# Kernel tuning notes

Measured on AMD Instinct MI355X. Metric: run time of the kernel, lower is better.

Reference implementation:

```python
import jax, jax.numpy as jnp
import numpy as np

N_HEADS = 64
N_KV = 8
HEAD_DIM = 128
HIDDEN = 8192
BATCH = 32
PAD_LEN = 2048  # nearest_32(start_pos + 1) with start_pos = 2047


def setup_inputs() -> dict:
    key = jax.random.key(0)
    ks = jax.random.split(key, 8)
    w = 0.02
    return {
        "x": jax.random.normal(ks[0], (BATCH, 1, HIDDEN), jnp.float32),
        "wq": jax.random.normal(ks[1], (HIDDEN, N_HEADS * HEAD_DIM), jnp.float32) * w,
        "wk": jax.random.normal(ks[2], (HIDDEN, N_KV * HEAD_DIM), jnp.float32) * w,
        "wv": jax.random.normal(ks[3], (HIDDEN, N_KV * HEAD_DIM), jnp.float32) * w,
        "wo": jax.random.normal(ks[4], (N_HEADS * HEAD_DIM, HIDDEN), jnp.float32) * w,
        "rot_mat": jax.random.normal(ks[5], (HEAD_DIM, HEAD_DIM), jnp.float32) * w,
        "k_cache": jax.random.normal(ks[6], (BATCH, N_KV, PAD_LEN, HEAD_DIM), jnp.float32),
        "v_cache": jax.random.normal(ks[7], (BATCH, N_KV, PAD_LEN, HEAD_DIM), jnp.float32),
        "start_pos": 2047,
    }


def reference(x, wq, wk, wv, wo, rot_mat, k_cache, v_cache, start_pos):
    B = x.shape[0]
    L = k_cache.shape[2]  # padded past length (nearest_32(start_pos+1))
    scale = 1.0 / np.sqrt(HEAD_DIM).astype(np.float32)

    xt = x[:, 0]  # [B, HIDDEN], seq_len == 1 (decode)
    # QKV projections + rotary applied via explicit matmul with rot_mat
    q = (xt @ wq).reshape(B, N_HEADS, HEAD_DIM) @ rot_mat      # [B, nH, d]
    k_new = (xt @ wk).reshape(B, N_KV, HEAD_DIM) @ rot_mat     # [B, nKV, d]
    v_new = (xt @ wv).reshape(B, N_KV, HEAD_DIM)               # [B, nKV, d]

    # in-place KV cache update at current position
    keys = k_cache.at[:, :, start_pos].set(k_new)              # [B, nKV, L, d]
    vals = v_cache.at[:, :, start_pos].set(v_new)

    # grouped (multi-query) attention: 8 q-heads per kv-head
    qg = q.reshape(B, N_KV, N_HEADS // N_KV, HEAD_DIM)         # [B, nKV, g, d]
    scores = jnp.einsum("bkgd,bkld->bkgl", qg, keys) * scale   # [B, nKV, g, L]
    # padded causal mask: positions beyond start_pos are masked with finfo.min
    mask = jnp.where(jnp.arange(L) > start_pos,
                     jnp.finfo(scores.dtype).min, 0.0).astype(scores.dtype)
    attn = jax.nn.softmax(scores + mask, axis=-1)
    out = jnp.einsum("bkgl,bkld->bkgd", attn, vals)            # [B, nKV, g, d]
    out = out.reshape(B, N_HEADS * HEAD_DIM) @ wo              # dense out-proj
    return out[:, None, :]                                     # [B, 1, HIDDEN]
```

## Files before the change

### kernel.cpp

```cpp
#include <hip/hip_runtime.h>
#include <hip/hip_bf16.h>

#define HIDDEN 8192
#define NHEADS 64
#define NKV 8
#define HD 128
#define BATCH 32
#define PADLEN 2048
#define NCHUNK 4
#define CHUNKLEN 512

using bf16x8 = __attribute__((ext_vector_type(8))) short;
using f32x4 = __attribute__((ext_vector_type(4))) float;

__device__ __forceinline__ void gld16(const float* g, float* l) {
    __builtin_amdgcn_global_load_lds(
        (const __attribute__((address_space(1))) void*)g,
        (__attribute__((address_space(3))) void*)l,
        16, 0, 0);
}

__device__ __forceinline__ float readlane_f(float v, int lane) {
    return __uint_as_float(__builtin_amdgcn_readlane(__float_as_uint(v), lane));
}

__device__ __forceinline__ short f2bf(float f) {
    unsigned u = __float_as_uint(f);
    u += 0x7fff + ((u >> 16) & 1);
    return (short)(u >> 16);
}
__device__ __forceinline__ float bf2f(short s) {
    return __uint_as_float(((unsigned)(unsigned short)s) << 16);
}

__global__ __launch_bounds__(256) void cvt_split(const float* __restrict__ in,
                                                 short* __restrict__ hi,
                                                 short* __restrict__ lo, int n4) {
    int i = blockIdx.x * 256 + threadIdx.x;
    if (i >= n4) return;
    float4 v = ((const float4*)in)[i];
    short4 h, l;
    h.x = f2bf(v.x); l.x = f2bf(v.x - bf2f(h.x));
    h.y = f2bf(v.y); l.y = f2bf(v.y - bf2f(h.y));
    h.z = f2bf(v.z); l.z = f2bf(v.z - bf2f(h.z));
    h.w = f2bf(v.w); l.w = f2bf(v.w - bf2f(h.w));
    ((short4*)hi)[i] = h;
    ((short4*)lo)[i] = l;
}

#define QSEC 262144
#define KSEC 294912
#define QKV_STRIDE 327680
#define NSPLIT 16
#define KSLICE 512

__global__ __launch_bounds__(256) void gemm_mfma(
        const short* __restrict__ xhi, const short* __restrict__ xlo,
        const float* __restrict__ W0, const float* __restrict__ W1,
        const float* __restrict__ W2, float* __restrict__ P, size_t pstride) {
    const int tid = threadIdx.x;
    const int wv = tid >> 6, ln = tid & 63;
    const int cb = blockIdx.x, kb = blockIdx.y;

    const float* W; int N2; size_t so; int nbase;
    if (cb < 64)      { W = W0; N2 = 8192; so = 0;    nbase = cb * 128; }
    else if (cb < 72) { W = W1; N2 = 1024; so = QSEC; nbase = (cb - 64) * 128; }
    else              { W = W2; N2 = 1024; so = KSEC; nbase = (cb - 72) * 128; }

    const int n0 = nbase + wv * 32;
    const int lrow = ln & 15;
    const int kgrp = ln >> 4;
    const int k0 = kb * KSLICE;

    const float* wp0 = W + (size_t)(k0 + kgrp * 8) * N2 + (n0 + lrow);
    const float* wp1 = wp0 + 16;
    const short* xh0 = xhi + (size_t)lrow * HIDDEN + k0 + kgrp * 8;
    const short* xl0 = xlo + (size_t)lrow * HIDDEN + k0 + kgrp * 8;
    const short* xh1 = xh0 + (size_t)16 * HIDDEN;
    const short* xl1 = xl0 + (size_t)16 * HIDDEN;

    f32x4 acc00 = {0.f,0.f,0.f,0.f}, acc01 = {0.f,0.f,0.f,0.f};
    f32x4 acc10 = {0.f,0.f,0.f,0.f}, acc11 = {0.f,0.f,0.f,0.f};

    float c0[8], c1[8], pb0[8], pb1[8];
    bf16x8 A0h, A0l, A1h, A1l, N0h, N0l, N1h, N1l;

    auto loadB = [&](int kk, float (&b0)[8], float (&b1)[8]) {
#pragma unroll
        for (int j = 0; j < 8; ++j) {
            b0[j] = wp0[(size_t)(kk + j) * N2];
            b1[j] = wp1[(size_t)(kk + j) * N2];
        }
    };
    auto loadA = [&](int kk, bf16x8& h0, bf16x8& l0, bf16x8& h1, bf16x8& l1) {
        h0 = *(const bf16x8*)(xh0 + kk);
        l0 = *(const bf16x8*)(xl0 + kk);
        h1 = *(const bf16x8*)(xh1 + kk);
        l1 = *(const bf16x8*)(xl1 + kk);
    };
    auto domfma = [&](float (&b0)[8], float (&b1)[8],
                      bf16x8 ah0, bf16x8 al0, bf16x8 ah1, bf16x8 al1) {
        bf16x8 bh0, bl0, bh1, bl1;
#pragma unroll
        for (int j = 0; j < 8; ++j) {
            short h0 = f2bf(b0[j]); bh0[j] = h0; bl0[j] = f2bf(b0[j] - bf2f(h0));
            short h1 = f2bf(b1[j]); bh1[j] = h1; bl1[j] = f2bf(b1[j] - bf2f(h1));
        }
        acc00 = __builtin_amdgcn_mfma_f32_16x16x32_bf16(ah0, bh0, acc00, 0, 0, 0);
        acc10 = __builtin_amdgcn_mfma_f32_16x16x32_bf16(ah1, bh0, acc10, 0, 0, 0);
        acc01 = __builtin_amdgcn_mfma_f32_16x16x32_bf16(ah0, bh1, acc01, 0, 0, 0);
        acc11 = __builtin_amdgcn_mfma_f32_16x16x32_bf16(ah1, bh1, acc11, 0, 0, 0);
        acc00 = __builtin_amdgcn_mfma_f32_16x16x32_bf16(al0, bh0, acc00, 0, 0, 0);
        acc10 = __builtin_amdgcn_mfma_f32_16x16x32_bf16(al1, bh0, acc10, 0, 0, 0);
        acc01 = __builtin_amdgcn_mfma_f32_16x16x32_bf16(al0, bh1, acc01, 0, 0, 0);
        acc11 = __builtin_amdgcn_mfma_f32_16x16x32_bf16(al1, bh1, acc11, 0, 0, 0);
        acc00 = __builtin_amdgcn_mfma_f32_16x16x32_bf16(ah0, bl0, acc00, 0, 0, 0);
        acc10 = __builtin_amdgcn_mfma_f32_16x16x32_bf16(ah1, bl0, acc10, 0, 0, 0);
        acc01 = __builtin_amdgcn_mfma_f32_16x16x32_bf16(ah0, bl1, acc01, 0, 0, 0);
        acc11 = __builtin_amdgcn_mfma_f32_16x16x32_bf16(ah1, bl1, acc11, 0, 0, 0);
    };

    loadB(0, c0, c1);
    loadA(0, A0h, A0l, A1h, A1l);
#pragma unroll
    for (int kk = 0; kk < KSLICE - 32; kk += 32) {
        loadB(kk + 32, pb0, pb1);
        loadA(kk + 32, N0h, N0l, N1h, N1l);
        domfma(c0, c1, A0h, A0l, A1h, A1l);
#pragma unroll
        for (int j = 0; j < 8; ++j) { c0[j] = pb0[j]; c1[j] = pb1[j]; }
        A0h = N0h; A0l = N0l; A1h = N1h; A1l = N1l;
    }
    domfma(c0, c1, A0h, A0l, A1h, A1l);

    float* pb = P + (size_t)kb * pstride + so;
#pragma unroll
    for (int r = 0; r < 4; ++r) {
        int row0 = kgrp * 4 + r;
        pb[(size_t)row0 * N2 + n0 + lrow]            = acc00[r];
        pb[(size_t)row0 * N2 + n0 + 16 + lrow]       = acc01[r];
        pb[(size_t)(row0 + 16) * N2 + n0 + lrow]      = acc10[r];
        pb[(size_t)(row0 + 16) * N2 + n0 + 16 + lrow] = acc11[r];
    }
}

__global__ __launch_bounds__(256) void reduce_split(const float* __restrict__ P,
                                                    float* __restrict__ out,
                                                    int nelem, size_t pstride) {
    int i = (blockIdx.x * 256 + threadIdx.x) * 4;
    if (i >= nelem) return;
    float4 a = *(const float4*)(P + i);
#pragma unroll 4
    for (int s = 1; s < NSPLIT; ++s) {
        float4 b = *(const float4*)(P + (size_t)s * pstride + i);
        a.x += b.x; a.y += b.y; a.z += b.z; a.w += b.w;
    }
    *(float4*)(out + i) = a;
}

#define RROWS 16
__global__ __launch_bounds__(128) void rotary_all(const float* __restrict__ qin,
                                                  const float* __restrict__ kin,
                                                  const float* __restrict__ rot,
                                                  float* __restrict__ qout,
                                                  float* __restrict__ kout) {
    __shared__ float rows[RROWS][HD];
    const int tid = threadIdx.x;
    const int row0 = blockIdx.x * RROWS;

    for (int i = tid; i < RROWS * (HD / 4); i += 128) {
        int r = i >> 5;
        int d4 = i & 31;
        int gr = row0 + r;
        const float* src = (gr < BATCH * NHEADS)
                               ? (qin + (size_t)gr * HD)
                               : (kin + (size_t)(gr - BATCH * NHEADS) * HD);
        *(float4*)&rows[r][d4 * 4] = *(const float4*)(src + d4 * 4);
    }
    __syncthreads();

    float acc[RROWS];
#pragma unroll
    for (int r = 0; r < RROWS; ++r) acc[r] = 0.f;

    for (int d4 = 0; d4 < HD; d4 += 4) {
        float r0 = rot[(size_t)(d4 + 0) * HD + tid];
        float r1 = rot[(size_t)(d4 + 1) * HD + tid];
        float r2 = rot[(size_t)(d4 + 2) * HD + tid];
        float r3 = rot[(size_t)(d4 + 3) * HD + tid];
#pragma unroll
        for (int r = 0; r < RROWS; ++r) {
            float4 xv = *(const float4*)&rows[r][d4];
            acc[r] = fmaf(xv.x, r0, acc[r]);
            acc[r] = fmaf(xv.y, r1, acc[r]);
            acc[r] = fmaf(xv.z, r2, acc[r]);
            acc[r] = fmaf(xv.w, r3, acc[r]);
        }
    }
#pragma unroll
    for (int r = 0; r < RROWS; ++r) {
        int gr = row0 + r;
        float* dst = (gr < BATCH * NHEADS)
                         ? (qout + (size_t)gr * HD)
                         : (kout + (size_t)(gr - BATCH * NHEADS) * HD);
        dst[tid] = acc[r];
    }
}

#define TILE 16
#define NBUF 4
__global__ __launch_bounds__(512, 4) void attn_decode(
        const float* __restrict__ qr, const float* __restrict__ kr,
        const float* __restrict__ vnew, const float* __restrict__ kcache,
        const float* __restrict__ vcache, const int* __restrict__ sp_ptr,
        float* __restrict__ part_acc, float* __restrict__ part_md) {
    __shared__ float4 kt[NBUF][TILE][32];
    __shared__ float4 vt[NBUF][TILE][32];

    const int tid = threadIdx.x;
    const int wv = tid >> 6, ln = tid & 63;
    const int row = ln & 15, qd = ln >> 4;
    const int dslot = ln & 31, hh = ln >> 5;
    const int chunk = blockIdx.x >> 8;
    const int b  = (blockIdx.x >> 3) & 31;
    const int kv = blockIdx.x & 7;
    const int chunk0 = chunk * CHUNKLEN;
    const int sp = sp_ptr[0];
    const float scale = 0.08838834764831845f;
    const int bh = b * NHEADS + kv * 8 + wv;

    const float* kbase = kcache + (size_t)(b * NKV + kv) * PADLEN * HD;
    const float* vbase = vcache + (size_t)(b * NKV + kv) * PADLEN * HD;
    const float* knew  = kr   + (size_t)(b * NKV + kv) * HD;
    const float* vnw   = vnew + (size_t)(b * NKV + kv) * HD;

    float4 qreg[8];
    {
        const float4* qsrc = (const float4*)(qr + (size_t)bh * HD) + qd * 8;
#pragma unroll
        for (int i = 0; i < 8; ++i) qreg[i] = qsrc[i];
    }

    const int sr  = wv * 2 + (ln >> 5);
    const int sj  = ln & 31;
    const int sjk = sj ^ (sr & 7);

    float m_run = -1e30f, dsum = 0.f;
    float4 acc = make_float4(0.f, 0.f, 0.f, 0.f);

    int valid = sp + 1 - chunk0;
    int nt = valid <= 0 ? 0 : (valid + TILE - 1) >> 4;
    if (nt > CHUNKLEN / TILE) nt = CHUNKLEN / TILE;

    auto stage = [&](int ts, int slot) {
        const int gl = chunk0 + (ts << 4) + sr;
        const float* krow = (gl == sp) ? knew : (kbase + (size_t)gl * HD);
        const float* vrow = (gl == sp) ? vnw  : (vbase + (size_t)gl * HD);
        gld16(krow + (sjk << 2), (float*)&kt[slot][0][0] + wv * 256);
        gld16(vrow + (sj  << 2), (float*)&vt[slot][0][0] + wv * 256);
    };

    auto compute = [&](int t) {
        const float4 (*kt_)[32] = kt[t & 3];
        const float4 (*vt_)[32] = vt[t & 3];
        float sh = 0.f;
#pragma unroll
        for (int jj = 0; jj < 8; ++jj) {
            float4 kk = kt_[row][(qd * 8 + jj) ^ (row & 7)];
            float4 qq = qreg[jj];
            sh = fmaf(qq.x, kk.x, sh);
            sh = fmaf(qq.y, kk.y, sh);
            sh = fmaf(qq.z, kk.z, sh);
            sh = fmaf(qq.w, kk.w, sh);
        }
        sh += __shfl_xor(sh, 16);
        sh += __shfl_xor(sh, 32);
        float s0 = sh * scale;
        const int l0 = chunk0 + (t << 4) + row;
        const bool dead = l0 > sp;
        if (dead) s0 = -1e30f;

        float mt = s0;
        mt = fmaxf(mt, __shfl_xor(mt, 1));
        mt = fmaxf(mt, __shfl_xor(mt, 2));
        mt = fmaxf(mt, __shfl_xor(mt, 4));
        mt = fmaxf(mt, __shfl_xor(mt, 8));
        float mnew = fmaxf(m_run, mt);
        float f = __expf(m_run - mnew);
        float p0 = dead ? 0.f : __expf(s0 - mnew);
        m_run = mnew;
        dsum = dsum * f + p0;
        acc.x *= f; acc.y *= f; acc.z *= f; acc.w *= f;

#pragma unroll
        for (int i = 0; i < 8; ++i) {
            float4 vv = vt_[hh * 8 + i][dslot];
            float pa = readlane_f(p0, i);
            float pb = readlane_f(p0, 8 + i);
            float pr = hh ? pb : pa;
            acc.x = fmaf(pr, vv.x, acc.x);
            acc.y = fmaf(pr, vv.y, acc.y);
            acc.z = fmaf(pr, vv.z, acc.z);
            acc.w = fmaf(pr, vv.w, acc.w);
        }
    };

    if (nt > 0) {
        stage(0, 0);
        stage(nt > 1 ? 1 : 0, 1);
        for (int t = 0; t < nt; ++t) {
            int ts = t + 2 < nt ? t + 2 : nt - 1;
            stage(ts, (t + 2) & 3);
            asm volatile("s_waitcnt vmcnt(4)" ::: "memory");
            __builtin_amdgcn_s_barrier();
            compute(t);
        }
    }

    acc.x += __shfl_xor(acc.x, 32);
    acc.y += __shfl_xor(acc.y, 32);
    acc.z += __shfl_xor(acc.z, 32);
    acc.w += __shfl_xor(acc.w, 32);
    float dd = dsum;
    dd += __shfl_xor(dd, 1);
    dd += __shfl_xor(dd, 2);
    dd += __shfl_xor(dd, 4);
    dd += __shfl_xor(dd, 8);

    if (hh == 0)
        *(float4*)(part_acc + ((size_t)chunk * (BATCH * NHEADS) + bh) * HD + dslot * 4) = acc;
    if (ln == 0) {
        float2 md = make_float2(m_run, dd);
        *(float2*)(part_md + ((size_t)chunk * (BATCH * NHEADS) + bh) * 2) = md;
    }
}

__global__ __launch_bounds__(128) void attn_combine(const float* __restrict__ part_acc,
                                                    const float* __restrict__ part_md,
                                                    float* __restrict__ attn_out) {
    const int bh = blockIdx.x;
    const int d = threadIdx.x;
    float m[NCHUNK], dd[NCHUNK];
    float M = -1e30f;
#pragma unroll
    for (int c = 0; c < NCHUNK; ++c) {
        m[c]  = part_md[((size_t)c * (BATCH * NHEADS) + bh) * 2];
        dd[c] = part_md[((size_t)c * (BATCH * NHEADS) + bh) * 2 + 1];
        M = fmaxf(M, m[c]);
    }
    float D = 0.f, o = 0.f;
#pragma unroll
    for (int c = 0; c < NCHUNK; ++c) {
        float w = __expf(m[c] - M);
        D += dd[c] * w;
        o += part_acc[((size_t)c * (BATCH * NHEADS) + bh) * HD + d] * w;
    }
    attn_out[(size_t)bh * HD + d] = o / D;
}

extern "C" void kernel_launch(void* const* d_in, const int* in_sizes, int n_in,
                              void* d_out, int out_size, void* d_ws, size_t ws_size,
                              hipStream_t stream) {
    const float* x   = (const float*)d_in[0];
    const float* wq  = (const float*)d_in[1];
    const float* wk  = (const float*)d_in[2];
    const float* wv  = (const float*)d_in[3];
    const float* wo  = (const float*)d_in[4];
    const float* rot = (const float*)d_in[5];
    const float* kc  = (const float*)d_in[6];
    const float* vc  = (const float*)d_in[7];
    const int*   sp  = (const int*)d_in[8];
    float* out = (float*)d_out;

    float* ws = (float*)d_ws;
    float* qkv_buf  = ws;
    float* q_buf    = qkv_buf;
    float* k_buf    = qkv_buf + QSEC;
    float* v_buf    = qkv_buf + KSEC;
    float* qr_buf   = ws + 327680;
    float* kr_buf   = ws + 589824;
    float* attn_buf = ws + 622592;
    short* xhi      = (short*)(ws + 884736);
    short* xlo      = (short*)(ws + 884736 + 131072);
    short* ahi      = (short*)(ws + 884736 + 262144);
    short* alo      = (short*)(ws + 884736 + 393216);
    float* P        = ws + 884736 + 524288;
    float* part_acc = P;
    float* part_md  = P + 1048576;

    cvt_split<<<(QSEC / 4 + 255) / 256, 256, 0, stream>>>(x, xhi, xlo, QSEC / 4);
    gemm_mfma<<<dim3(80, NSPLIT), 256, 0, stream>>>(xhi, xlo, wq, wk, wv, P, QKV_STRIDE);
    reduce_split<<<(QKV_STRIDE / 4 + 255) / 256, 256, 0, stream>>>(
        P, qkv_buf, QKV_STRIDE, QKV_STRIDE);

    rotary_all<<<(BATCH * NHEADS + BATCH * NKV) / RROWS, 128, 0, stream>>>(
        q_buf, k_buf, rot, qr_buf, kr_buf);

    attn_decode<<<NCHUNK * BATCH * NKV, 512, 0, stream>>>(
        qr_buf, kr_buf, v_buf, kc, vc, sp, part_acc, part_md);
    attn_combine<<<BATCH * NHEADS, 128, 0, stream>>>(part_acc, part_md, attn_buf);

    cvt_split<<<(QSEC / 4 + 255) / 256, 256, 0, stream>>>(attn_buf, ahi, alo, QSEC / 4);
    gemm_mfma<<<dim3(64, NSPLIT), 256, 0, stream>>>(ahi, alo, wo, wo, wo, P, QSEC);
    reduce_split<<<(QSEC / 4 + 255) / 256, 256, 0, stream>>>(P, out, QSEC, QSEC);
}
```

Before: 302.5 us.

## Fuse split-K reduce into rotary, fuse combine with bf16 split, stream V directly

Merges the QKV split-K reduction into the rotary kernel, which also writes V, and folds the bf16 hi/lo conversion into the attention combine kernel. Together these remove two launches and their intermediate round trips through global memory. In attention decode, V tiles are no longer staged into LDS; each lane reads V straight from global memory. This halves LDS use and allows raising the occupancy hint to 8 blocks. The direct V loads are strided per row and no longer overlap with compute through the async pipeline, which may expose latency.

```diff
diff --git a/kernel.cpp b/kernel.cpp
--- a/kernel.cpp
+++ b/kernel.cpp
@@ -137,8 +137,8 @@
 #pragma unroll
     for (int r = 0; r < 4; ++r) {
         int row0 = kgrp * 4 + r;
-        pb[(size_t)row0 * N2 + n0 + lrow]            = acc00[r];
-        pb[(size_t)row0 * N2 + n0 + 16 + lrow]       = acc01[r];
+        pb[(size_t)row0 * N2 + n0 + lrow]             = acc00[r];
+        pb[(size_t)row0 * N2 + n0 + 16 + lrow]        = acc01[r];
         pb[(size_t)(row0 + 16) * N2 + n0 + lrow]      = acc10[r];
         pb[(size_t)(row0 + 16) * N2 + n0 + 16 + lrow] = acc11[r];
     }
@@ -159,63 +159,80 @@
 }
 
 #define RROWS 16
-__global__ __launch_bounds__(128) void rotary_all(const float* __restrict__ qin,
-                                                  const float* __restrict__ kin,
-                                                  const float* __restrict__ rot,
-                                                  float* __restrict__ qout,
-                                                  float* __restrict__ kout) {
+__global__ __launch_bounds__(128) void reduce_rotary(const float* __restrict__ P,
+                                                     const float* __restrict__ rot,
+                                                     float* __restrict__ qout,
+                                                     float* __restrict__ kout,
+                                                     float* __restrict__ vout) {
     __shared__ float rows[RROWS][HD];
     const int tid = threadIdx.x;
-    const int row0 = blockIdx.x * RROWS;
-
-    for (int i = tid; i < RROWS * (HD / 4); i += 128) {
-        int r = i >> 5;
-        int d4 = i & 31;
-        int gr = row0 + r;
-        const float* src = (gr < BATCH * NHEADS)
-                               ? (qin + (size_t)gr * HD)
-                               : (kin + (size_t)(gr - BATCH * NHEADS) * HD);
-        *(float4*)&rows[r][d4 * 4] = *(const float4*)(src + d4 * 4);
-    }
-    __syncthreads();
-
-    float acc[RROWS];
-#pragma unroll
-    for (int r = 0; r < RROWS; ++r) acc[r] = 0.f;
-
-    for (int d4 = 0; d4 < HD; d4 += 4) {
-        float r0 = rot[(size_t)(d4 + 0) * HD + tid];
-        float r1 = rot[(size_t)(d4 + 1) * HD + tid];
-        float r2 = rot[(size_t)(d4 + 2) * HD + tid];
-        float r3 = rot[(size_t)(d4 + 3) * HD + tid];
+    const int blk = blockIdx.x;
+
+    if (blk < 144) {
+        const int row0 = blk * RROWS;
+        for (int i = tid; i < RROWS * HD; i += 128) {
+            int r = row0 + (i >> 7);
+            int d = i & 127;
+            size_t off;
+            if (r < BATCH * NHEADS) off = (size_t)(r >> 6) * 8192 + (r & 63) * 128 + d;
+            else {
+                int r2 = r - BATCH * NHEADS;
+                off = QSEC + (size_t)(r2 >> 3) * 1024 + (r2 & 7) * 128 + d;
+            }
+            float a = P[off];
+#pragma unroll 5
+            for (int s = 1; s < NSPLIT; ++s) a += P[(size_t)s * QKV_STRIDE + off];
+            rows[i >> 7][d] = a;
+        }
+        __syncthreads();
+
+        float acc[RROWS];
+#pragma unroll
+        for (int r = 0; r < RROWS; ++r) acc[r] = 0.f;
+        for (int d4 = 0; d4 < HD; d4 += 4) {
+            float r0 = rot[(size_t)(d4 + 0) * HD + tid];
+            float r1 = rot[(size_t)(d4 + 1) * HD + tid];
+            float r2 = rot[(size_t)(d4 + 2) * HD + tid];
+            float r3 = rot[(size_t)(d4 + 3) * HD + tid];
+#pragma unroll
+            for (int r = 0; r < RROWS; ++r) {
+                float4 xv = *(const float4*)&rows[r][d4];
+                acc[r] = fmaf(xv.x, r0, acc[r]);
+                acc[r] = fmaf(xv.y, r1, acc[r]);
+                acc[r] = fmaf(xv.z, r2, acc[r]);
+                acc[r] = fmaf(xv.w, r3, acc[r]);
+            }
+        }
 #pragma unroll
         for (int r = 0; r < RROWS; ++r) {
-            float4 xv = *(const float4*)&rows[r][d4];
-            acc[r] = fmaf(xv.x, r0, acc[r]);
-            acc[r] = fmaf(xv.y, r1, acc[r]);
-            acc[r] = fmaf(xv.z, r2, acc[r]);
-            acc[r] = fmaf(xv.w, r3, acc[r]);
-        }
-    }
-#pragma unroll
-    for (int r = 0; r < RROWS; ++r) {
-        int gr = row0 + r;
-        float* dst = (gr < BATCH * NHEADS)
-                         ? (qout + (size_t)gr * HD)
-                         : (kout + (size_t)(gr - BATCH * NHEADS) * HD);
-        dst[tid] = acc[r];
+            int gr = row0 + r;
+            float* dst = (gr < BATCH * NHEADS)
+                             ? (qout + (size_t)gr * HD)
+                             : (kout + (size_t)(gr - BATCH * NHEADS) * HD);
+            dst[tid] = acc[r];
+        }
+    } else {
+        const int row0 = (blk - 144) * RROWS;
+        for (int i = tid; i < RROWS * HD; i += 128) {
+            int r2 = row0 + (i >> 7);
+            int d = i & 127;
+            size_t off = KSEC + (size_t)(r2 >> 3) * 1024 + (r2 & 7) * 128 + d;
+            float a = P[off];
+#pragma unroll 5
+            for (int s = 1; s < NSPLIT; ++s) a += P[(size_t)s * QKV_STRIDE + off];
+            vout[(size_t)r2 * HD + d] = a;
+        }
     }
 }
 
 #define TILE 16
 #define NBUF 4
-__global__ __launch_bounds__(512, 4) void attn_decode(
+__global__ __launch_bounds__(512, 8) void attn_decode(
         const float* __restrict__ qr, const float* __restrict__ kr,
         const float* __restrict__ vnew, const float* __restrict__ kcache,
         const float* __restrict__ vcache, const int* __restrict__ sp_ptr,
         float* __restrict__ part_acc, float* __restrict__ part_md) {
     __shared__ float4 kt[NBUF][TILE][32];
-    __shared__ float4 vt[NBUF][TILE][32];
 
     const int tid = threadIdx.x;
     const int wv = tid >> 6, ln = tid & 63;
@@ -255,14 +272,12 @@
     auto stage = [&](int ts, int slot) {
         const int gl = chunk0 + (ts << 4) + sr;
         const float* krow = (gl == sp) ? knew : (kbase + (size_t)gl * HD);
-        const float* vrow = (gl == sp) ? vnw  : (vbase + (size_t)gl * HD);
         gld16(krow + (sjk << 2), (float*)&kt[slot][0][0] + wv * 256);
-        gld16(vrow + (sj  << 2), (float*)&vt[slot][0][0] + wv * 256);
     };
 
     auto compute = [&](int t) {
         const float4 (*kt_)[32] = kt[t & 3];
-        const float4 (*vt_)[32] = vt[t & 3];
+        const int tile0 = chunk0 + (t << 4);
         float sh = 0.f;
 #pragma unroll
         for (int jj = 0; jj < 8; ++jj) {
@@ -276,7 +291,7 @@
         sh += __shfl_xor(sh, 16);
         sh += __shfl_xor(sh, 32);
         float s0 = sh * scale;
-        const int l0 = chunk0 + (t << 4) + row;
+        const int l0 = tile0 + row;
         const bool dead = l0 > sp;
         if (dead) s0 = -1e30f;
 
@@ -294,7 +309,9 @@
 
 #pragma unroll
         for (int i = 0; i < 8; ++i) {
-            float4 vv = vt_[hh * 8 + i][dslot];
+            int gl = tile0 + hh * 8 + i;
+            const float* vr = (gl == sp) ? vnw : (vbase + (size_t)gl * HD);
+            float4 vv = *(const float4*)(vr + dslot * 4);
             float pa = readlane_f(p0, i);
             float pb = readlane_f(p0, 8 + i);
             float pr = hh ? pb : pa;
@@ -311,7 +328,7 @@
         for (int t = 0; t < nt; ++t) {
             int ts = t + 2 < nt ? t + 2 : nt - 1;
             stage(ts, (t + 2) & 3);
-            asm volatile("s_waitcnt vmcnt(4)" ::: "memory");
+            asm volatile("s_waitcnt vmcnt(2)" ::: "memory");
             __builtin_amdgcn_s_barrier();
             compute(t);
         }
@@ -335,9 +352,9 @@
     }
 }
 
-__global__ __launch_bounds__(128) void attn_combine(const float* __restrict__ part_acc,
-                                                    const float* __restrict__ part_md,
-                                                    float* __restrict__ attn_out) {
+__global__ __launch_bounds__(128) void attn_combine_cvt(
+        const float* __restrict__ part_acc, const float* __restrict__ part_md,
+        short* __restrict__ ahi, short* __restrict__ alo) {
     const int bh = blockIdx.x;
     const int d = threadIdx.x;
     float m[NCHUNK], dd[NCHUNK];
@@ -355,7 +372,10 @@
         D += dd[c] * w;
         o += part_acc[((size_t)c * (BATCH * NHEADS) + bh) * HD + d] * w;
     }
-    attn_out[(size_t)bh * HD + d] = o / D;
+    float v = o / D;
+    short h = f2bf(v);
+    ahi[(size_t)bh * HD + d] = h;
+    alo[(size_t)bh * HD + d] = f2bf(v - bf2f(h));
 }
 
 extern "C" void kernel_launch(void* const* d_in, const int* in_sizes, int n_in,
@@ -373,13 +393,9 @@
     float* out = (float*)d_out;
 
     float* ws = (float*)d_ws;
-    float* qkv_buf  = ws;
-    float* q_buf    = qkv_buf;
-    float* k_buf    = qkv_buf + QSEC;
-    float* v_buf    = qkv_buf + KSEC;
+    float* v_buf    = ws;
     float* qr_buf   = ws + 327680;
     float* kr_buf   = ws + 589824;
-    float* attn_buf = ws + 622592;
     short* xhi      = (short*)(ws + 884736);
     short* xlo      = (short*)(ws + 884736 + 131072);
     short* ahi      = (short*)(ws + 884736 + 262144);
@@ -390,17 +406,12 @@
 
     cvt_split<<<(QSEC / 4 + 255) / 256, 256, 0, stream>>>(x, xhi, xlo, QSEC / 4);
     gemm_mfma<<<dim3(80, NSPLIT), 256, 0, stream>>>(xhi, xlo, wq, wk, wv, P, QKV_STRIDE);
-    reduce_split<<<(QKV_STRIDE / 4 + 255) / 256, 256, 0, stream>>>(
-        P, qkv_buf, QKV_STRIDE, QKV_STRIDE);
-
-    rotary_all<<<(BATCH * NHEADS + BATCH * NKV) / RROWS, 128, 0, stream>>>(
-        q_buf, k_buf, rot, qr_buf, kr_buf);
+    reduce_rotary<<<160, 128, 0, stream>>>(P, rot, qr_buf, kr_buf, v_buf);
 
     attn_decode<<<NCHUNK * BATCH * NKV, 512, 0, stream>>>(
         qr_buf, kr_buf, v_buf, kc, vc, sp, part_acc, part_md);
-    attn_combine<<<BATCH * NHEADS, 128, 0, stream>>>(part_acc, part_md, attn_buf);
-
-    cvt_split<<<(QSEC / 4 + 255) / 256, 256, 0, stream>>>(attn_buf, ahi, alo, QSEC / 4);
+    attn_combine_cvt<<<BATCH * NHEADS, 128, 0, stream>>>(part_acc, part_md, ahi, alo);
+
     gemm_mfma<<<dim3(64, NSPLIT), 256, 0, stream>>>(ahi, alo, wo, wo, wo, P, QSEC);
     reduce_split<<<(QSEC / 4 + 255) / 256, 256, 0, stream>>>(P, out, QSEC, QSEC);
 }
```

After: 474.1 us. 1.57x slower.
